# Performance work log

Measured on AMD Instinct MI355X. Metric: run time of the kernel, lower is better.

Reference implementation:

```python
import jax, jax.numpy as jnp
import numpy as np
from jax import lax

IN_PLANES = 512
GROWTH = 32
PLANES = 4 * GROWTH  # 128
EPS = 1e-5


def setup_inputs() -> dict:
    key = jax.random.key(0)
    ks = jax.random.split(key, 10)
    x = jax.random.normal(ks[0], (128, IN_PLANES, 32, 32), dtype=jnp.float32)
    # bn1 affine params (batch-stat BN, track_running_stats=False)
    gamma1 = jax.random.normal(ks[1], (IN_PLANES,), dtype=jnp.float32) * 0.1 + 1.0
    beta1 = jax.random.normal(ks[2], (IN_PLANES,), dtype=jnp.float32) * 0.1
    # convbn1: 1x1 conv weight + folded BN (running stats)
    w1 = jax.random.normal(ks[3], (PLANES, IN_PLANES, 1, 1), dtype=jnp.float32) * (1.0 / np.sqrt(IN_PLANES))
    gamma2 = jax.random.normal(ks[4], (PLANES,), dtype=jnp.float32) * 0.1 + 1.0
    beta2 = jax.random.normal(ks[5], (PLANES,), dtype=jnp.float32) * 0.1
    mean2 = jax.random.normal(ks[6], (PLANES,), dtype=jnp.float32) * 0.1
    var2 = jax.random.uniform(ks[7], (PLANES,), dtype=jnp.float32, minval=0.5, maxval=1.5)
    # conv2: 3x3 conv, padding 1, no bias
    w2 = jax.random.normal(ks[8], (GROWTH, PLANES, 3, 3), dtype=jnp.float32) * (1.0 / np.sqrt(9 * PLANES))
    return {"x": x, "gamma1": gamma1, "beta1": beta1, "w1": w1,
            "gamma2": gamma2, "beta2": beta2, "mean2": mean2, "var2": var2,
            "w2": w2}


def _bn(h, mean, var, gamma, beta):
    # channel-wise affine normalization, NCHW
    inv = lax.rsqrt(var + EPS)
    scale = (gamma * inv)[None, :, None, None]
    shift = (beta - mean * gamma * inv)[None, :, None, None]
    return h * scale + shift


def reference(x, gamma1, beta1, w1, gamma2, beta2, mean2, var2, w2):
    # bn1: batch statistics (track_running_stats=False)
    mu = jnp.mean(x, axis=(0, 2, 3))
    var = jnp.var(x, axis=(0, 2, 3))  # biased, as torch BN normalization
    h = _bn(x, mu, var, gamma1, beta1)
    h = jax.nn.relu(h)
    # convbn1: 1x1 conv then folded BN (running stats)
    h = lax.conv_general_dilated(h, w1, (1, 1), 'VALID',
                                 dimension_numbers=('NCHW', 'OIHW', 'NCHW'))
    h = _bn(h, mean2, var2, gamma2, beta2)
    h = jax.nn.relu(h)
    # conv2: 3x3, stride 1, pad 1, no bias
    out = lax.conv_general_dilated(h, w2, (1, 1), ((1, 1), (1, 1)),
                                   dimension_numbers=('NCHW', 'OIHW', 'NCHW'))
    # dense concat along channels
    return jnp.concatenate([x, out], axis=1)
```

## Files before the change

kernel.cpp:

```cpp
#include <hip/hip_runtime.h>

#define EPS 1e-5f

typedef __bf16 bf16x8 __attribute__((ext_vector_type(8)));
typedef __bf16 bf16x4 __attribute__((ext_vector_type(4)));
typedef unsigned short ushort8 __attribute__((ext_vector_type(8)));
typedef float f32x4 __attribute__((ext_vector_type(4)));

static __device__ __forceinline__ unsigned short f2bf(float f) {
  unsigned int u = __float_as_uint(f);
  u += 0x7fffu + ((u >> 16) & 1u);
  return (unsigned short)(u >> 16);
}


__global__ void __launch_bounds__(256) k1_kernel(
    const float* __restrict__ x, float* __restrict__ out,
    float* __restrict__ psum, float* __restrict__ psq,
    const float* __restrict__ w1, const float* __restrict__ gamma2,
    const float* __restrict__ beta2, const float* __restrict__ mean2,
    const float* __restrict__ var2, const float* __restrict__ w2,
    unsigned short* __restrict__ w1b, unsigned short* __restrict__ w2b,
    float* __restrict__ bias2) {
  const int t = threadIdx.x;
  if (blockIdx.x >= 4096) {
    int idx = (blockIdx.x - 4096) * 256 + t;
    if (idx < 128 * 512) {
      int oc = idx >> 9;
      float s2 = gamma2[oc] * rsqrtf(var2[oc] + EPS);
      w1b[idx] = f2bf(w1[idx] * s2);
    } else if (idx < 128 * 512 + 32 * 1152) {
      int i2 = idx - 128 * 512;
      int oc = i2 / 1152;
      int rem = i2 - oc * 1152;
      int tap = rem >> 7;
      int c = rem & 127;
      w2b[i2] = f2bf(w2[(oc * 128 + c) * 9 + tap]);
    } else if (idx < 128 * 512 + 32 * 1152 + 128) {
      int oc = idx - (128 * 512 + 32 * 1152);
      float s2 = gamma2[oc] * rsqrtf(var2[oc] + EPS);
      bias2[oc] = beta2[oc] - mean2[oc] * s2;
    }
    return;
  }
  const int c = blockIdx.x & 511;
  const int nq = blockIdx.x >> 9;
  float sum = 0.f, sq = 0.f;
  const f32x4* __restrict__ x4 = (const f32x4*)x;
  f32x4* out4 = (f32x4*)out;
#pragma unroll 8
  for (int i = 0; i < 16; ++i) {
    const int n = nq * 16 + i;
    f32x4 v = x4[(((size_t)n * 512 + c) << 8) + t];
    __builtin_nontemporal_store(v, &out4[(((size_t)n * 544 + c) << 8) + t]);
    sum += v[0] + v[1] + v[2] + v[3];
    sq += v[0] * v[0] + v[1] * v[1] + v[2] * v[2] + v[3] * v[3];
  }
  __shared__ float ls[2][4];
  for (int off = 32; off > 0; off >>= 1) {
    sum += __shfl_down(sum, off);
    sq += __shfl_down(sq, off);
  }
  const int w = t >> 6;
  if ((t & 63) == 0) { ls[0][w] = sum; ls[1][w] = sq; }
  __syncthreads();
  if (t == 0) {
    psum[c * 8 + nq] = ls[0][0] + ls[0][1] + ls[0][2] + ls[0][3];
    psq[c * 8 + nq] = ls[1][0] + ls[1][1] + ls[1][2] + ls[1][3];
  }
}

__global__ void __launch_bounds__(256, 2) conv1_kernel(
    const float* __restrict__ x, const unsigned short* __restrict__ w1b,
    const float* __restrict__ psum, const float* __restrict__ psq,
    const float* __restrict__ g1, const float* __restrict__ be1,
    const float* __restrict__ bias2, unsigned short* __restrict__ h2) {
  const int t = threadIdx.x;
  __shared__ float s1s[512], b1s[512];
  __shared__ __align__(16) unsigned short tile0[32 * 260];
  __shared__ __align__(16) unsigned short tile1[32 * 260];

  for (int cc = t; cc < 512; cc += 256) {
    float S = 0.f, Q = 0.f;
#pragma unroll
    for (int qq = 0; qq < 8; ++qq) { S += psum[cc * 8 + qq]; Q += psq[cc * 8 + qq]; }
    float mean = S * (1.0f / 131072.0f);
    float var = Q * (1.0f / 131072.0f) - mean * mean;
    float s = g1[cc] * rsqrtf(var + EPS);
    s1s[cc] = s;
    b1s[cc] = be1[cc] - mean * s;
  }
  __syncthreads();

  const int lane = t & 63;
  const int wv = t >> 6;
  const int n = 127 - (blockIdx.x >> 2);
  const int q = blockIdx.x & 3;
  const int l15 = lane & 15;
  const int kb = lane >> 4;

  f32x4 acc[8][4];
#pragma unroll
  for (int m = 0; m < 8; ++m)
#pragma unroll
    for (int g = 0; g < 4; ++g) acc[m][g] = (f32x4){0.f, 0.f, 0.f, 0.f};

  const f32x4* __restrict__ xq = (const f32x4*)(x + (size_t)n * 524288 + q * 256);

  f32x4 va[8], vb[8];

#define LOADV(vv, kk)                                               \
  {                                                                 \
    _Pragma("unroll") for (int i = 0; i < 8; ++i)                   \
        vv[i] = xq[(size_t)((kk) * 32 + wv * 8 + i) * 256 + lane];  \
  }
#define STAGE(tl, kk, vv)                                              \
  {                                                                    \
    _Pragma("unroll") for (int i = 0; i < 8; ++i) {                    \
      const int c = (kk) * 32 + wv * 8 + i;                            \
      const float s = s1s[c], b = b1s[c];                              \
      bf16x4 bv;                                                       \
      bv[0] = (__bf16)fmaxf(fmaf(vv[i][0], s, b), 0.f);                \
      bv[1] = (__bf16)fmaxf(fmaf(vv[i][1], s, b), 0.f);                \
      bv[2] = (__bf16)fmaxf(fmaf(vv[i][2], s, b), 0.f);                \
      bv[3] = (__bf16)fmaxf(fmaf(vv[i][3], s, b), 0.f);                \
      *(bf16x4*)&tl[(size_t)(wv * 8 + i) * 260 + 4 * lane] = bv;       \
    }                                                                  \
  }
#define FRAGMFMA(tl, kk)                                                    \
  {                                                                         \
    bf16x8 bf[4];                                                           \
    _Pragma("unroll") for (int g = 0; g < 4; ++g) {                         \
      const int pl = wv * 64 + g * 16 + l15;                                \
      bf16x8 tmp;                                                           \
      _Pragma("unroll") for (int j = 0; j < 8; ++j)                         \
          tmp[j] = __builtin_bit_cast(__bf16, tl[(kb * 8 + j) * 260 + pl]); \
      bf[g] = tmp;                                                          \
    }                                                                       \
    _Pragma("unroll") for (int m = 0; m < 8; ++m) {                         \
      bf16x8 af =                                                           \
          *(const bf16x8*)(w1b + (size_t)(m * 16 + l15) * 512 + (kk) * 32 + \
                           kb * 8);                                         \
      _Pragma("unroll") for (int g = 0; g < 4; ++g) acc[m][g] =             \
          __builtin_amdgcn_mfma_f32_16x16x32_bf16(af, bf[g], acc[m][g], 0,  \
                                                  0, 0);                    \
    }                                                                       \
  }

  LOADV(va, 0);
  STAGE(tile0, 0, va);
  LOADV(va, 1);
  __syncthreads();

  for (int k2 = 0; k2 < 8; ++k2) {
    const int ke = 2 * k2, ko = 2 * k2 + 1;
    STAGE(tile1, ke + 1, va);
    if (ke + 2 < 16) LOADV(vb, ke + 2);
    FRAGMFMA(tile0, ke);
    __syncthreads();
    if (ko + 1 < 16) {
      STAGE(tile0, ko + 1, vb);
      LOADV(va, ko + 2);
    }
    FRAGMFMA(tile1, ko);
    __syncthreads();
  }
#undef LOADV
#undef STAGE
#undef FRAGMFMA

#pragma unroll
  for (int m = 0; m < 8; ++m) {
    const int ocb = m * 16 + kb * 4;
    float bz0 = bias2[ocb + 0], bz1 = bias2[ocb + 1];
    float bz2 = bias2[ocb + 2], bz3 = bias2[ocb + 3];
#pragma unroll
    for (int g = 0; g < 4; ++g) {
      const int p = q * 256 + wv * 64 + g * 16 + l15;
      bf16x4 hv;
      hv[0] = (__bf16)fmaxf(acc[m][g][0] + bz0, 0.f);
      hv[1] = (__bf16)fmaxf(acc[m][g][1] + bz1, 0.f);
      hv[2] = (__bf16)fmaxf(acc[m][g][2] + bz2, 0.f);
      hv[3] = (__bf16)fmaxf(acc[m][g][3] + bz3, 0.f);
      *(bf16x4*)(h2 + ((size_t)n * 1024 + p) * 128 + ocb) = hv;
    }
  }
}

__global__ void __launch_bounds__(256) conv2_kernel(
    const unsigned short* __restrict__ h2, const unsigned short* __restrict__ w2b,
    float* __restrict__ out) {
  const int t = threadIdx.x;
  const int lane = t & 63;
  const int wv = t >> 6;
  const int n = blockIdx.x >> 3;
  const int pbase = (blockIdx.x & 7) * 128 + wv * 32;
  const int l15 = lane & 15;
  const int kb = lane >> 4;

  f32x4 acc[2][2];
#pragma unroll
  for (int m = 0; m < 2; ++m)
#pragma unroll
    for (int g = 0; g < 2; ++g) acc[m][g] = (f32x4){0.f, 0.f, 0.f, 0.f};

  const unsigned short* __restrict__ h2n = h2 + (size_t)n * 1024 * 128;

#pragma unroll
  for (int tap = 0; tap < 9; ++tap) {
    const int dy = tap / 3 - 1;
    const int dx = tap % 3 - 1;
#pragma unroll
    for (int c0 = 0; c0 < 128; c0 += 32) {
      const int cb = c0 + kb * 8;
      bf16x8 af[2];
#pragma unroll
      for (int m = 0; m < 2; ++m)
        af[m] = *(const bf16x8*)(w2b + (size_t)(m * 16 + l15) * 1152 + tap * 128 + cb);
#pragma unroll
      for (int g = 0; g < 2; ++g) {
        const int p = pbase + g * 16 + l15;
        const int y = (p >> 5) & 31;
        const int xx = p & 31;
        const int y2 = y + dy;
        const int x2 = xx + dx;
        bf16x8 bv = __builtin_bit_cast(bf16x8, (ushort8){0, 0, 0, 0, 0, 0, 0, 0});
        if (y2 >= 0 && y2 < 32 && x2 >= 0 && x2 < 32)
          bv = *(const bf16x8*)(h2n + ((size_t)(y2 * 32 + x2)) * 128 + cb);
#pragma unroll
        for (int m = 0; m < 2; ++m)
          acc[m][g] = __builtin_amdgcn_mfma_f32_16x16x32_bf16(af[m], bv, acc[m][g], 0, 0, 0);
      }
    }
  }

#pragma unroll
  for (int m = 0; m < 2; ++m) {
    const int oc = m * 16 + kb * 4;
#pragma unroll
    for (int g = 0; g < 2; ++g) {
      const int p = pbase + g * 16 + l15;
#pragma unroll
      for (int r = 0; r < 4; ++r)
        __builtin_nontemporal_store(
            acc[m][g][r], &out[((size_t)n * 544 + 512 + oc + r) * 1024 + p]);
    }
  }
}

extern "C" void kernel_launch(void* const* d_in, const int* in_sizes, int n_in,
                              void* d_out, int out_size, void* d_ws, size_t ws_size,
                              hipStream_t stream) {
  const float* x = (const float*)d_in[0];
  const float* gamma1 = (const float*)d_in[1];
  const float* beta1 = (const float*)d_in[2];
  const float* w1 = (const float*)d_in[3];
  const float* gamma2 = (const float*)d_in[4];
  const float* beta2 = (const float*)d_in[5];
  const float* mean2 = (const float*)d_in[6];
  const float* var2 = (const float*)d_in[7];
  const float* w2 = (const float*)d_in[8];
  float* out = (float*)d_out;

  char* ws = (char*)d_ws;
  unsigned short* h2 = (unsigned short*)ws;
  unsigned short* w1b = (unsigned short*)(ws + 33554432);
  unsigned short* w2b = (unsigned short*)(ws + 33685504);
  float* bias2 = (float*)(ws + 33759232);
  float* psum = (float*)(ws + 33763840);
  float* psq = (float*)(ws + 33780224);

  k1_kernel<<<4497, 256, 0, stream>>>(x, out, psum, psq,
                                      w1, gamma2, beta2, mean2, var2, w2,
                                      w1b, w2b, bias2);
  conv1_kernel<<<512, 256, 0, stream>>>(x, w1b, psum, psq, gamma1, beta1,
                                        bias2, h2);
  conv2_kernel<<<1024, 256, 0, stream>>>(h2, w2b, out);
}
```

Baseline: 247.4 us.

## Split BN stat reduction into its own kernel, single-buffer conv1, widen conv2 tiles

```diff
diff --git a/kernel.cpp b/kernel.cpp
--- a/kernel.cpp
+++ b/kernel.cpp
@@ -70,25 +70,34 @@
   }
 }
 
+__global__ void reduce_kernel(const float* __restrict__ psum,
+                              const float* __restrict__ psq,
+                              const float* __restrict__ g1,
+                              const float* __restrict__ be1,
+                              float* __restrict__ s1, float* __restrict__ b1) {
+  int c = blockIdx.x * 256 + threadIdx.x;
+  if (c < 512) {
+    float S = 0.f, Q = 0.f;
+#pragma unroll
+    for (int q = 0; q < 8; ++q) { S += psum[c * 8 + q]; Q += psq[c * 8 + q]; }
+    float mean = S * (1.0f / 131072.0f);
+    float var = Q * (1.0f / 131072.0f) - mean * mean;
+    float s = g1[c] * rsqrtf(var + EPS);
+    s1[c] = s;
+    b1[c] = be1[c] - mean * s;
+  }
+}
+
 __global__ void __launch_bounds__(256, 2) conv1_kernel(
     const float* __restrict__ x, const unsigned short* __restrict__ w1b,
-    const float* __restrict__ psum, const float* __restrict__ psq,
-    const float* __restrict__ g1, const float* __restrict__ be1,
+    const float* __restrict__ s1, const float* __restrict__ b1,
     const float* __restrict__ bias2, unsigned short* __restrict__ h2) {
   const int t = threadIdx.x;
   __shared__ float s1s[512], b1s[512];
-  __shared__ __align__(16) unsigned short tile0[32 * 260];
-  __shared__ __align__(16) unsigned short tile1[32 * 260];
-
+  __shared__ __align__(16) unsigned short tile[32 * 260];
   for (int cc = t; cc < 512; cc += 256) {
-    float S = 0.f, Q = 0.f;
-#pragma unroll
-    for (int qq = 0; qq < 8; ++qq) { S += psum[cc * 8 + qq]; Q += psq[cc * 8 + qq]; }
-    float mean = S * (1.0f / 131072.0f);
-    float var = Q * (1.0f / 131072.0f) - mean * mean;
-    float s = g1[cc] * rsqrtf(var + EPS);
-    s1s[cc] = s;
-    b1s[cc] = be1[cc] - mean * s;
+    s1s[cc] = s1[cc];
+    b1s[cc] = b1[cc];
   }
   __syncthreads();
 
@@ -109,12 +118,12 @@
 
   f32x4 va[8], vb[8];
 
-#define LOADV(vv, kk)                                               \
-  {                                                                 \
-    _Pragma("unroll") for (int i = 0; i < 8; ++i)                   \
-        vv[i] = xq[(size_t)((kk) * 32 + wv * 8 + i) * 256 + lane];  \
-  }
-#define STAGE(tl, kk, vv)                                              \
+#define LOADV(vv, kk)                                                \
+  {                                                                  \
+    _Pragma("unroll") for (int i = 0; i < 8; ++i)                    \
+        vv[i] = xq[(size_t)((kk) * 32 + wv * 8 + i) * 256 + lane];   \
+  }
+#define STAGE(kk, vv)                                                  \
   {                                                                    \
     _Pragma("unroll") for (int i = 0; i < 8; ++i) {                    \
       const int c = (kk) * 32 + wv * 8 + i;                            \
@@ -124,23 +133,22 @@
       bv[1] = (__bf16)fmaxf(fmaf(vv[i][1], s, b), 0.f);                \
       bv[2] = (__bf16)fmaxf(fmaf(vv[i][2], s, b), 0.f);                \
       bv[3] = (__bf16)fmaxf(fmaf(vv[i][3], s, b), 0.f);                \
-      *(bf16x4*)&tl[(size_t)(wv * 8 + i) * 260 + 4 * lane] = bv;       \
+      *(bf16x4*)&tile[(size_t)(wv * 8 + i) * 260 + 4 * lane] = bv;     \
     }                                                                  \
   }
-#define FRAGMFMA(tl, kk)                                                    \
+#define FRAGMFMA(kk)                                                        \
   {                                                                         \
     bf16x8 bf[4];                                                           \
     _Pragma("unroll") for (int g = 0; g < 4; ++g) {                         \
       const int pl = wv * 64 + g * 16 + l15;                                \
       bf16x8 tmp;                                                           \
       _Pragma("unroll") for (int j = 0; j < 8; ++j)                         \
-          tmp[j] = __builtin_bit_cast(__bf16, tl[(kb * 8 + j) * 260 + pl]); \
+          tmp[j] = __builtin_bit_cast(__bf16, tile[(kb * 8 + j) * 260 + pl]); \
       bf[g] = tmp;                                                          \
     }                                                                       \
     _Pragma("unroll") for (int m = 0; m < 8; ++m) {                         \
-      bf16x8 af =                                                           \
-          *(const bf16x8*)(w1b + (size_t)(m * 16 + l15) * 512 + (kk) * 32 + \
-                           kb * 8);                                         \
+      bf16x8 af = *(const bf16x8*)(w1b + (size_t)(m * 16 + l15) * 512 +     \
+                                   (kk) * 32 + kb * 8);                     \
       _Pragma("unroll") for (int g = 0; g < 4; ++g) acc[m][g] =             \
           __builtin_amdgcn_mfma_f32_16x16x32_bf16(af, bf[g], acc[m][g], 0,  \
                                                   0, 0);                    \
@@ -148,21 +156,19 @@
   }
 
   LOADV(va, 0);
-  STAGE(tile0, 0, va);
-  LOADV(va, 1);
-  __syncthreads();
+  LOADV(vb, 1);
 
   for (int k2 = 0; k2 < 8; ++k2) {
     const int ke = 2 * k2, ko = 2 * k2 + 1;
-    STAGE(tile1, ke + 1, va);
-    if (ke + 2 < 16) LOADV(vb, ke + 2);
-    FRAGMFMA(tile0, ke);
-    __syncthreads();
-    if (ko + 1 < 16) {
-      STAGE(tile0, ko + 1, vb);
-      LOADV(va, ko + 2);
-    }
-    FRAGMFMA(tile1, ko);
+    STAGE(ke, va);
+    if (ke + 2 < 16) LOADV(va, ke + 2);
+    __syncthreads();
+    FRAGMFMA(ke);
+    __syncthreads();
+    STAGE(ko, vb);
+    if (ko + 2 < 16) LOADV(vb, ko + 2);
+    __syncthreads();
+    FRAGMFMA(ko);
     __syncthreads();
   }
 #undef LOADV
@@ -193,16 +199,16 @@
   const int t = threadIdx.x;
   const int lane = t & 63;
   const int wv = t >> 6;
-  const int n = blockIdx.x >> 3;
-  const int pbase = (blockIdx.x & 7) * 128 + wv * 32;
+  const int n = blockIdx.x >> 2;
+  const int pbase = (blockIdx.x & 3) * 256 + wv * 64;
   const int l15 = lane & 15;
   const int kb = lane >> 4;
 
-  f32x4 acc[2][2];
+  f32x4 acc[2][4];
 #pragma unroll
   for (int m = 0; m < 2; ++m)
 #pragma unroll
-    for (int g = 0; g < 2; ++g) acc[m][g] = (f32x4){0.f, 0.f, 0.f, 0.f};
+    for (int g = 0; g < 4; ++g) acc[m][g] = (f32x4){0.f, 0.f, 0.f, 0.f};
 
   const unsigned short* __restrict__ h2n = h2 + (size_t)n * 1024 * 128;
 
@@ -218,7 +224,7 @@
       for (int m = 0; m < 2; ++m)
         af[m] = *(const bf16x8*)(w2b + (size_t)(m * 16 + l15) * 1152 + tap * 128 + cb);
 #pragma unroll
-      for (int g = 0; g < 2; ++g) {
+      for (int g = 0; g < 4; ++g) {
         const int p = pbase + g * 16 + l15;
         const int y = (p >> 5) & 31;
         const int xx = p & 31;
@@ -238,7 +244,7 @@
   for (int m = 0; m < 2; ++m) {
     const int oc = m * 16 + kb * 4;
 #pragma unroll
-    for (int g = 0; g < 2; ++g) {
+    for (int g = 0; g < 4; ++g) {
       const int p = pbase + g * 16 + l15;
 #pragma unroll
       for (int r = 0; r < 4; ++r)
@@ -267,13 +273,15 @@
   unsigned short* w1b = (unsigned short*)(ws + 33554432);
   unsigned short* w2b = (unsigned short*)(ws + 33685504);
   float* bias2 = (float*)(ws + 33759232);
+  float* s1 = (float*)(ws + 33759744);
+  float* b1 = (float*)(ws + 33761792);
   float* psum = (float*)(ws + 33763840);
   float* psq = (float*)(ws + 33780224);
 
   k1_kernel<<<4497, 256, 0, stream>>>(x, out, psum, psq,
                                       w1, gamma2, beta2, mean2, var2, w2,
                                       w1b, w2b, bias2);
-  conv1_kernel<<<512, 256, 0, stream>>>(x, w1b, psum, psq, gamma1, beta1,
-                                        bias2, h2);
-  conv2_kernel<<<1024, 256, 0, stream>>>(h2, w2b, out);
-}
+  reduce_kernel<<<2, 256, 0, stream>>>(psum, psq, gamma1, beta1, s1, b1);
+  conv1_kernel<<<512, 256, 0, stream>>>(x, w1b, s1, b1, bias2, h2);
+  conv2_kernel<<<512, 256, 0, stream>>>(h2, w2b, out);
+}
```

Measured after the change: 229.0 us. 7.4% less time.
